# Optimization experiments

Measured on AMD Instinct MI355X. Metric: run time of the kernel, lower is better.

Reference implementation:

```python
import jax, jax.numpy as jnp
import numpy as np

B, S, D = 8, 4096, 1024


def setup_inputs() -> dict:
    key = jax.random.key(0)
    kq, kk, kv, kw, kb = jax.random.split(key, 5)
    query = jax.random.normal(kq, (B, S, D), dtype=jnp.float32)
    k = jax.random.normal(kk, (B, S, D), dtype=jnp.float32)
    value = jax.random.normal(kv, (B, S, D), dtype=jnp.float32)
    # nn.Linear(hidden_size, hidden_size) params (Kaiming-uniform-ish init scale)
    bound = 1.0 / np.sqrt(D)
    W_out = jax.random.uniform(kw, (D, D), minval=-bound, maxval=bound, dtype=jnp.float32)
    b_out = jax.random.uniform(kb, (D,), minval=-bound, maxval=bound, dtype=jnp.float32)
    return {"query": query, "key": k, "value": value, "W_out": W_out, "b_out": b_out}


def reference(query, key, value, W_out, b_out):
    d = query.shape[-1]
    scale = 1.0 / jnp.sqrt(jnp.asarray(d, dtype=query.dtype))
    # scores: [B, Sq, Sk]
    scores = jnp.einsum("bqd,bkd->bqk", query, key) * scale
    attn = jax.nn.softmax(scores, axis=-1)
    # training=False -> dropout is identity
    ctx = jnp.einsum("bqk,bkd->bqd", attn, value)
    # nn.Linear: x @ W^T + b
    out = jnp.einsum("bqd,ed->bqe", ctx, W_out) + b_out
    return out
```

## Files before the change

### kernel.cpp

```cpp
#include <hip/hip_runtime.h>
#include <hip/hip_bf16.h>

typedef __attribute__((ext_vector_type(4))) float f4;
typedef __attribute__((ext_vector_type(4))) short s4;
typedef __attribute__((ext_vector_type(8))) short s8;

#define SEQ 4096
#define DIM 1024
#define NB 8

__device__ inline short f2bf(float f) {
    return __builtin_bit_cast(short, __float2bfloat16(f));
}

__device__ inline float bf2f(short s) {
    return __builtin_bit_cast(float, (unsigned)((unsigned short)s) << 16);
}

__device__ inline void gload_lds16(const void* g, void* l) {
    __builtin_amdgcn_global_load_lds(
        (const __attribute__((address_space(1))) void*)g,
        (__attribute__((address_space(3))) void*)l, 16, 0, 0);
}

template<int OUT>
__global__ __launch_bounds__(512, 2) void gemm256(
    const short* __restrict__ A, size_t lda, size_t bsA,
    const short* __restrict__ B, size_t ldb, size_t bsB,
    void* __restrict__ C, size_t ldc, size_t bsC,
    const float* __restrict__ bias, int nt, int gridN)
{
    __shared__ short lds[2 * 32768];
    const int tid  = threadIdx.x;
    const int lane = tid & 63;
    const int wave = tid >> 6;

    A += (size_t)blockIdx.y * bsA;
    B += (size_t)blockIdx.y * bsB;
    float* Cf = (float*)C + (size_t)blockIdx.y * bsC;
    short* Cs = (short*)C + (size_t)blockIdx.y * bsC;

    const int nwg = gridDim.x;
    int wg = blockIdx.x;
    wg = (wg & 7) * (nwg >> 3) + (wg >> 3);
    const size_t tm = (size_t)(wg / gridN) * 256;
    const size_t tn = (size_t)(wg % gridN) * 256;

    const int srow = tid >> 3;
    const int slot = tid & 7;
    const int sc   = slot ^ (srow & 7);
    const short* pA = A + (tm + srow) * lda + sc * 8;
    const short* pB = B + (tn + srow) * ldb + sc * 8;
    const int ldst = srow * 64 + slot * 8;

    const int fr = lane & 15, kg = lane >> 4;
    const int wr = wave >> 2, wc = wave & 3;

    auto STAGE = [&](int t) {
        short* bufA = lds + (t & 1) * 32768;
        short* bufB = bufA + 16384;
        const size_t k0 = (size_t)t * 64;
        #pragma unroll
        for (int j = 0; j < 4; ++j) {
            gload_lds16(pA + (size_t)(j * 64) * lda + k0, bufA + j * 4096 + ldst);
            gload_lds16(pB + (size_t)(j * 64) * ldb + k0, bufB + j * 4096 + ldst);
        }
    };

    f4 acc[8][4];
    #pragma unroll
    for (int m = 0; m < 8; ++m)
        #pragma unroll
        for (int n = 0; n < 4; ++n)
            acc[m][n] = (f4){0.f, 0.f, 0.f, 0.f};

    STAGE(0);
    __syncthreads();

    for (int t = 0; t < nt; ++t) {
        if (t + 1 < nt) STAGE(t + 1);

        const short* bufA = lds + (t & 1) * 32768;
        const short* bufB = bufA + 16384;
        s8 af[2][8], bf[2][4];
        #pragma unroll
        for (int kh = 0; kh < 2; ++kh) {
            #pragma unroll
            for (int m = 0; m < 8; ++m) {
                const int row = wr * 128 + m * 16 + fr;
                const int c   = kh * 4 + kg;
                af[kh][m] = *(const s8*)(bufA + row * 64 + (c ^ (row & 7)) * 8);
            }
            #pragma unroll
            for (int n = 0; n < 4; ++n) {
                const int row = wc * 64 + n * 16 + fr;
                const int c   = kh * 4 + kg;
                bf[kh][n] = *(const s8*)(bufB + row * 64 + (c ^ (row & 7)) * 8);
            }
        }
        __builtin_amdgcn_s_setprio(1);
        #pragma unroll
        for (int kh = 0; kh < 2; ++kh)
            #pragma unroll
            for (int m = 0; m < 8; ++m)
                #pragma unroll
                for (int n = 0; n < 4; ++n)
                    acc[m][n] = __builtin_amdgcn_mfma_f32_16x16x32_bf16(
                        af[kh][m], bf[kh][n], acc[m][n], 0, 0, 0);
        __builtin_amdgcn_s_setprio(0);

        __syncthreads();
    }

    const int cg = lane >> 4, cl = lane & 15;
    #pragma unroll
    for (int m = 0; m < 8; ++m) {
        #pragma unroll
        for (int n = 0; n < 4; ++n) {
            const size_t grow = tm + wr * 128 + m * 16 + cg * 4;
            const size_t gcol = tn + wc * 64 + n * 16 + cl;
            float bv = 0.f;
            if constexpr (OUT == 0) { if (bias) bv = bias[gcol]; }
            #pragma unroll
            for (int i = 0; i < 4; ++i) {
                const float val = acc[m][n][i] + bv;
                if constexpr (OUT == 0)
                    Cf[(grow + i) * ldc + gcol] = val;
                else
                    Cs[(grow + i) * ldc + gcol] = f2bf(val);
            }
        }
    }
}

__global__ __launch_bounds__(256) void conv_bf16(const float* __restrict__ in,
                                                 short* __restrict__ out, int n8)
{
    const int i = blockIdx.x * 256 + threadIdx.x;
    if (i >= n8) return;
    f4 a = ((const f4*)in)[2 * i];
    f4 b = ((const f4*)in)[2 * i + 1];
    s8 w;
    w[0] = f2bf(a[0]); w[1] = f2bf(a[1]); w[2] = f2bf(a[2]); w[3] = f2bf(a[3]);
    w[4] = f2bf(b[0]); w[5] = f2bf(b[1]); w[6] = f2bf(b[2]); w[7] = f2bf(b[3]);
    ((s8*)out)[i] = w;
}

__global__ __launch_bounds__(256) void prep_batch4(
    const float* __restrict__ Q4, const float* __restrict__ K4,
    const float* __restrict__ V4,
    short* __restrict__ Qb4, short* __restrict__ Kb4, short* __restrict__ VT4)
{
    const int tid = threadIdx.x;
    const int b4  = blockIdx.x >> 13;
    const int blk = blockIdx.x & 8191;
    const size_t io = (size_t)b4 * SEQ * DIM;

    if (blk < 4096) {
        const float* in = ((blk < 2048) ? Q4 : K4) + io;
        short* out      = ((blk < 2048) ? Qb4 : Kb4) + io;
        const int i = (blk & 2047) * 256 + tid;
        f4 a = ((const f4*)in)[2 * i];
        f4 b = ((const f4*)in)[2 * i + 1];
        s8 w;
        w[0] = f2bf(a[0]); w[1] = f2bf(a[1]); w[2] = f2bf(a[2]); w[3] = f2bf(a[3]);
        w[4] = f2bf(b[0]); w[5] = f2bf(b[1]); w[6] = f2bf(b[2]); w[7] = f2bf(b[3]);
        ((s8*)out)[i] = w;
    } else {
        __shared__ float t[32][33];
        const float* Vf = V4 + io;
        short* VT = VT4 + (size_t)b4 * DIM * SEQ;
        const int b2 = blk - 4096;
        const size_t k0 = (size_t)(b2 & 127) * 32;
        const size_t d0 = (size_t)(b2 >> 7) * 32;

        const int r = tid >> 3, c4 = (tid & 7) * 4;
        f4 x = *(const f4*)(Vf + (k0 + r) * DIM + d0 + c4);
        #pragma unroll
        for (int i = 0; i < 4; ++i) t[r][c4 + i] = x[i];
        __syncthreads();

        const int d = tid >> 3, kk = (tid & 7) * 4;
        s4 w;
        #pragma unroll
        for (int i = 0; i < 4; ++i) w[i] = f2bf(t[kk + i][d]);
        *(s4*)(VT + (d0 + d) * SEQ + k0 + kk) = w;
    }
}

__global__ __launch_bounds__(256) void prep_batch(
    const float* __restrict__ Qf, const float* __restrict__ Kf,
    const float* __restrict__ Vf,
    short* __restrict__ Qb, short* __restrict__ Kb, short* __restrict__ VT)
{
    const int tid = threadIdx.x;
    const int blk = blockIdx.x;

    if (blk < 4096) {
        const float* in = (blk < 2048) ? Qf : Kf;
        short* out      = (blk < 2048) ? Qb : Kb;
        const int i = (blk & 2047) * 256 + tid;
        f4 a = ((const f4*)in)[2 * i];
        f4 b = ((const f4*)in)[2 * i + 1];
        s8 w;
        w[0] = f2bf(a[0]); w[1] = f2bf(a[1]); w[2] = f2bf(a[2]); w[3] = f2bf(a[3]);
        w[4] = f2bf(b[0]); w[5] = f2bf(b[1]); w[6] = f2bf(b[2]); w[7] = f2bf(b[3]);
        ((s8*)out)[i] = w;
    } else {
        __shared__ float t[32][33];
        const int b2 = blk - 4096;
        const size_t k0 = (size_t)(b2 & 127) * 32;
        const size_t d0 = (size_t)(b2 >> 7) * 32;

        const int r = tid >> 3, c4 = (tid & 7) * 4;
        f4 x = *(const f4*)(Vf + (k0 + r) * DIM + d0 + c4);
        #pragma unroll
        for (int i = 0; i < 4; ++i) t[r][c4 + i] = x[i];
        __syncthreads();

        const int d = tid >> 3, kk = (tid & 7) * 4;
        s4 w;
        #pragma unroll
        for (int i = 0; i < 4; ++i) w[i] = f2bf(t[kk + i][d]);
        *(s4*)(VT + (d0 + d) * SEQ + k0 + kk) = w;
    }
}

__global__ __launch_bounds__(256) void softmax_rows_bf(short* __restrict__ scores)
{
    const int tid = threadIdx.x;
    short* srow = scores + (size_t)blockIdx.y * SEQ * SEQ + (size_t)blockIdx.x * SEQ;
    const float SCALE = 0.03125f;

    float v[16];
    float mx = -3.4e38f;
    #pragma unroll
    for (int j = 0; j < 4; ++j) {
        s4 h = *(const s4*)(srow + (size_t)(j * 256 + tid) * 4);
        #pragma unroll
        for (int i = 0; i < 4; ++i) {
            const float f = bf2f(h[i]) * SCALE;
            v[j * 4 + i] = f;
            mx = fmaxf(mx, f);
        }
    }
    #pragma unroll
    for (int o = 32; o > 0; o >>= 1) mx = fmaxf(mx, __shfl_xor(mx, o));
    __shared__ float red[4];
    if ((tid & 63) == 0) red[tid >> 6] = mx;
    __syncthreads();
    mx = fmaxf(fmaxf(red[0], red[1]), fmaxf(red[2], red[3]));

    float sum = 0.f;
    #pragma unroll
    for (int j = 0; j < 16; ++j) {
        const float e = __expf(v[j] - mx);
        v[j] = e;
        sum += e;
    }
    #pragma unroll
    for (int o = 32; o > 0; o >>= 1) sum += __shfl_xor(sum, o);
    __syncthreads();
    if ((tid & 63) == 0) red[tid >> 6] = sum;
    __syncthreads();
    const float inv = 1.f / (red[0] + red[1] + red[2] + red[3]);

    #pragma unroll
    for (int j = 0; j < 4; ++j) {
        s4 w;
        #pragma unroll
        for (int i = 0; i < 4; ++i) w[i] = f2bf(v[j * 4 + i] * inv);
        *(s4*)(srow + (size_t)(j * 256 + tid) * 4) = w;
    }
}

extern "C" void kernel_launch(void* const* d_in, const int* in_sizes, int n_in,
                              void* d_out, int out_size, void* d_ws, size_t ws_size,
                              hipStream_t stream) {
    const float* Q    = (const float*)d_in[0];
    const float* Km   = (const float*)d_in[1];
    const float* V    = (const float*)d_in[2];
    const float* W    = (const float*)d_in[3];
    const float* bias = (const float*)d_in[4];
    float* out = (float*)d_out;

    const dim3 blk256(256), blk512(512);
    const size_t needBig =
        (size_t)NB * SEQ * DIM * 2 + (size_t)4 * DIM * SEQ * 2 +
        (size_t)4 * SEQ * DIM * 2 + (size_t)4 * SEQ * DIM * 2 +
        (size_t)DIM * DIM * 2;
    short* scoresB = (short*)d_out;

    if (ws_size >= needBig) {
        short* ctx = (short*)d_ws;
        short* VT4 = ctx + (size_t)NB * SEQ * DIM;
        short* Qb4 = VT4 + (size_t)4 * DIM * SEQ;
        short* Kb4 = Qb4 + (size_t)4 * SEQ * DIM;
        short* Wb  = Kb4 + (size_t)4 * SEQ * DIM;

        conv_bf16<<<DIM * DIM / 2048, blk256, 0, stream>>>(W, Wb, DIM * DIM / 8);

        for (int g = 0; g < 2; ++g) {
            const size_t go = (size_t)g * 4 * SEQ * DIM;
            prep_batch4<<<dim3(4 * 8192), blk256, 0, stream>>>(
                Q + go, Km + go, V + go, Qb4, Kb4, VT4);

            gemm256<2><<<dim3(256, 4), blk512, 0, stream>>>(
                Qb4, DIM, (size_t)SEQ * DIM,
                Kb4, DIM, (size_t)SEQ * DIM,
                scoresB, SEQ, (size_t)SEQ * SEQ,
                nullptr, DIM / 64, 16);

            softmax_rows_bf<<<dim3(SEQ, 4), blk256, 0, stream>>>(scoresB);

            gemm256<2><<<dim3(64, 4), blk512, 0, stream>>>(
                scoresB, SEQ, (size_t)SEQ * SEQ,
                VT4, SEQ, (size_t)DIM * SEQ,
                ctx + go, DIM, (size_t)SEQ * DIM,
                nullptr, SEQ / 64, 4);
        }
        gemm256<0><<<dim3(512, 1), blk512, 0, stream>>>(
            ctx, DIM, 0, Wb, DIM, 0, out, DIM, 0, bias, DIM / 64, 4);
    } else {
        short* ctx = (short*)d_ws;
        short* VT4 = ctx + (size_t)NB * SEQ * DIM;
        short* Qb  = VT4 + (size_t)4 * DIM * SEQ;
        short* Kb  = Qb + (size_t)SEQ * DIM;
        short* Wb  = Kb + (size_t)SEQ * DIM;

        conv_bf16<<<DIM * DIM / 2048, blk256, 0, stream>>>(W, Wb, DIM * DIM / 8);

        for (int g = 0; g < 2; ++g) {
            for (int b4 = 0; b4 < 4; ++b4) {
                const int b = g * 4 + b4;
                const float* Qf = Q  + (size_t)b * SEQ * DIM;
                const float* Kf = Km + (size_t)b * SEQ * DIM;
                const float* Vf = V  + (size_t)b * SEQ * DIM;

                prep_batch<<<dim3(8192), blk256, 0, stream>>>(
                    Qf, Kf, Vf, Qb, Kb, VT4 + (size_t)b4 * DIM * SEQ);

                gemm256<2><<<dim3(256, 1), blk512, 0, stream>>>(
                    Qb, DIM, 0, Kb, DIM, 0,
                    scoresB + (size_t)b4 * SEQ * SEQ, SEQ, 0,
                    nullptr, DIM / 64, 16);
            }
            softmax_rows_bf<<<dim3(SEQ, 4), blk256, 0, stream>>>(scoresB);

            gemm256<2><<<dim3(64, 4), blk512, 0, stream>>>(
                scoresB, SEQ, (size_t)SEQ * SEQ,
                VT4, SEQ, (size_t)DIM * SEQ,
                ctx + (size_t)g * 4 * SEQ * DIM, DIM, (size_t)SEQ * DIM,
                nullptr, SEQ / 64, 4);
        }
        gemm256<0><<<dim3(512, 1), blk512, 0, stream>>>(
            ctx, DIM, 0, Wb, DIM, 0, out, DIM, 0, bias, DIM / 64, 4);
    }
}
```

Before: 774.4 us.

## Restructure GEMM mainloop into 4-stage half-K pipeline with split A/B prefetch

The 256x256 bf16 GEMM mainloop moves from a double-buffered 64-wide K step to a four-slot ring of 32-wide K half-steps, prefetching three stages ahead. A and B loads are issued at different points in each iteration, and explicit vmcnt/lgkmcnt waits plus barriers interleave LDS fragment reads with MFMA bursts. The LDS layout drops the XOR swizzle and uses a row-major chunk-per-thread layout, so bank conflicts may increase. The aim is to hide global-to-LDS latency and overlap LDS reads with matrix math, at the cost of more barriers per K step.

Result: slower. 1.000 ms (+29.2%).

```diff
diff --git a/kernel.cpp b/kernel.cpp
--- a/kernel.cpp
+++ b/kernel.cpp
@@ -30,7 +30,7 @@
     void* __restrict__ C, size_t ldc, size_t bsC,
     const float* __restrict__ bias, int nt, int gridN)
 {
-    __shared__ short lds[2 * 32768];
+    __shared__ short lds[4 * 16384];
     const int tid  = threadIdx.x;
     const int lane = tid & 63;
     const int wave = tid >> 6;
@@ -46,25 +46,29 @@
     const size_t tm = (size_t)(wg / gridN) * 256;
     const size_t tn = (size_t)(wg % gridN) * 256;
 
-    const int srow = tid >> 3;
-    const int slot = tid & 7;
-    const int sc   = slot ^ (srow & 7);
-    const short* pA = A + (tm + srow) * lda + sc * 8;
-    const short* pB = B + (tn + srow) * ldb + sc * 8;
-    const int ldst = srow * 64 + slot * 8;
+    const int strow = tid & 127;
+    const int schnk = tid >> 7;
+    const short* pA = A + (tm + strow) * lda + schnk * 8;
+    const short* pB = B + (tn + strow) * ldb + schnk * 8;
+    const size_t a128 = (size_t)128 * lda;
+    const size_t b128 = (size_t)128 * ldb;
 
     const int fr = lane & 15, kg = lane >> 4;
     const int wr = wave >> 2, wc = wave & 3;
 
-    auto STAGE = [&](int t) {
-        short* bufA = lds + (t & 1) * 32768;
-        short* bufB = bufA + 16384;
-        const size_t k0 = (size_t)t * 64;
-        #pragma unroll
-        for (int j = 0; j < 4; ++j) {
-            gload_lds16(pA + (size_t)(j * 64) * lda + k0, bufA + j * 4096 + ldst);
-            gload_lds16(pB + (size_t)(j * 64) * ldb + k0, bufB + j * 4096 + ldst);
-        }
+    const int HMAX2 = 2 * nt;
+
+    auto STAGE_A = [&](int h) {
+        short* base = lds + (h & 3) * 16384;
+        const size_t k0 = (size_t)(h >> 1) * 64 + (size_t)(h & 1) * 32;
+        gload_lds16(pA + k0,        base + tid * 8);
+        gload_lds16(pA + a128 + k0, base + 4096 + tid * 8);
+    };
+    auto STAGE_B = [&](int h) {
+        short* base = lds + (h & 3) * 16384 + 8192;
+        const size_t k0 = (size_t)(h >> 1) * 64 + (size_t)(h & 1) * 32;
+        gload_lds16(pB + k0,        base + tid * 8);
+        gload_lds16(pB + b128 + k0, base + 4096 + tid * 8);
     };
 
     f4 acc[8][4];
@@ -74,42 +78,69 @@
         for (int n = 0; n < 4; ++n)
             acc[m][n] = (f4){0.f, 0.f, 0.f, 0.f};
 
-    STAGE(0);
-    __syncthreads();
-
-    for (int t = 0; t < nt; ++t) {
-        if (t + 1 < nt) STAGE(t + 1);
-
-        const short* bufA = lds + (t & 1) * 32768;
-        const short* bufB = bufA + 16384;
-        s8 af[2][8], bf[2][4];
-        #pragma unroll
-        for (int kh = 0; kh < 2; ++kh) {
+    STAGE_A(0); STAGE_B(0);
+    STAGE_A(1); STAGE_B(1);
+    STAGE_A(2); STAGE_B(2);
+    asm volatile("s_waitcnt vmcnt(8)" ::: "memory");
+    __builtin_amdgcn_s_barrier();
+    __builtin_amdgcn_sched_barrier(0);
+
+    for (int H = 0; H < HMAX2; ++H) {
+        const short* sA = lds + (H & 3) * 16384 + wr * 4096 + kg * 1024;
+        const short* sB = lds + (H & 3) * 16384 + 8192 + (wc >> 1) * 4096 + kg * 1024;
+        const int brow0 = (wc & 1) * 64;
+
+        s8 bf[4], af[4];
+        #pragma unroll
+        for (int n = 0; n < 4; ++n)
+            bf[n] = *(const s8*)(sB + (brow0 + n * 16 + fr) * 8);
+        #pragma unroll
+        for (int m = 0; m < 4; ++m)
+            af[m] = *(const s8*)(sA + (m * 16 + fr) * 8);
+        if (H + 3 < HMAX2) STAGE_A(H + 3);
+
+        __builtin_amdgcn_s_barrier();
+        asm volatile("s_waitcnt lgkmcnt(0)" ::: "memory");
+        __builtin_amdgcn_sched_barrier(0);
+        __builtin_amdgcn_s_setprio(1);
+        #pragma unroll
+        for (int m = 0; m < 4; ++m)
             #pragma unroll
-            for (int m = 0; m < 8; ++m) {
-                const int row = wr * 128 + m * 16 + fr;
-                const int c   = kh * 4 + kg;
-                af[kh][m] = *(const s8*)(bufA + row * 64 + (c ^ (row & 7)) * 8);
+            for (int n = 0; n < 4; ++n)
+                acc[m][n] = __builtin_amdgcn_mfma_f32_16x16x32_bf16(
+                    af[m], bf[n], acc[m][n], 0, 0, 0);
+        __builtin_amdgcn_s_setprio(0);
+        __builtin_amdgcn_s_barrier();
+
+        s8 ag[4];
+        #pragma unroll
+        for (int m = 0; m < 4; ++m)
+            ag[m] = *(const s8*)(sA + ((m + 4) * 16 + fr) * 8);
+        if (H + 3 < HMAX2) STAGE_B(H + 3);
+
+        __builtin_amdgcn_s_barrier();
+        asm volatile("s_waitcnt lgkmcnt(0)" ::: "memory");
+        __builtin_amdgcn_sched_barrier(0);
+        __builtin_amdgcn_s_setprio(1);
+        #pragma unroll
+        for (int m = 0; m < 4; ++m)
+            #pragma unroll
+            for (int n = 0; n < 4; ++n)
+                acc[m + 4][n] = __builtin_amdgcn_mfma_f32_16x16x32_bf16(
+                    ag[m], bf[n], acc[m + 4][n], 0, 0, 0);
+        __builtin_amdgcn_s_setprio(0);
+
+        if (H + 1 < HMAX2) {
+            if (H + 3 < HMAX2) {
+                asm volatile("s_waitcnt vmcnt(8)" ::: "memory");
+            } else if (H + 2 < HMAX2) {
+                asm volatile("s_waitcnt vmcnt(4)" ::: "memory");
+            } else {
+                asm volatile("s_waitcnt vmcnt(0)" ::: "memory");
             }
-            #pragma unroll
-            for (int n = 0; n < 4; ++n) {
-                const int row = wc * 64 + n * 16 + fr;
-                const int c   = kh * 4 + kg;
-                bf[kh][n] = *(const s8*)(bufB + row * 64 + (c ^ (row & 7)) * 8);
-            }
-        }
-        __builtin_amdgcn_s_setprio(1);
-        #pragma unroll
-        for (int kh = 0; kh < 2; ++kh)
-            #pragma unroll
-            for (int m = 0; m < 8; ++m)
-                #pragma unroll
-                for (int n = 0; n < 4; ++n)
-                    acc[m][n] = __builtin_amdgcn_mfma_f32_16x16x32_bf16(
-                        af[kh][m], bf[kh][n], acc[m][n], 0, 0, 0);
-        __builtin_amdgcn_s_setprio(0);
-
-        __syncthreads();
+            __builtin_amdgcn_s_barrier();
+            __builtin_amdgcn_sched_barrier(0);
+        }
     }
 
     const int cg = lane >> 4, cl = lane & 15;
@@ -333,12 +364,10 @@
         for (int g = 0; g < 2; ++g) {
             for (int b4 = 0; b4 < 4; ++b4) {
                 const int b = g * 4 + b4;
-                const float* Qf = Q  + (size_t)b * SEQ * DIM;
-                const float* Kf = Km + (size_t)b * SEQ * DIM;
-                const float* Vf = V  + (size_t)b * SEQ * DIM;
-
                 prep_batch<<<dim3(8192), blk256, 0, stream>>>(
-                    Qf, Kf, Vf, Qb, Kb, VT4 + (size_t)b4 * DIM * SEQ);
+                    Q + (size_t)b * SEQ * DIM, Km + (size_t)b * SEQ * DIM,
+                    V + (size_t)b * SEQ * DIM,
+                    Qb, Kb, VT4 + (size_t)b4 * DIM * SEQ);
 
                 gemm256<2><<<dim3(256, 1), blk512, 0, stream>>>(
                     Qb, DIM, 0, Kb, DIM, 0,
```
